# Performance work log

Measured on AMD Instinct MI355X. Metric: run time of the kernel, lower is better.

## Reference

```python
import jax, jax.numpy as jnp
import numpy as np

B, N, D = 8, 2048, 3
HIDDEN = (64, 128, 256)
LATENT = 128


def _layernorm(x, scale, bias, eps=1e-6):
    mu = jnp.mean(x, axis=-1, keepdims=True)
    var = jnp.mean((x - mu) ** 2, axis=-1, keepdims=True)
    return (x - mu) / jnp.sqrt(var + eps) * scale + bias


def setup_inputs() -> dict:
    key = jax.random.key(0)
    ks = jax.random.split(key, 8)
    inp = {
        "x": jax.random.normal(ks[0], (B, N, D), dtype=jnp.float32),
        "mask": jnp.ones((B, N), dtype=jnp.float32),
    }
    in_d = D
    for i, d in enumerate(HIDDEN):
        inp[f"W{i}"] = (jax.random.normal(ks[1 + i], (in_d, d), dtype=jnp.float32)
                        / np.float32(np.sqrt(in_d)))
        inp[f"b{i}"] = jnp.zeros((d,), dtype=jnp.float32)
        inp[f"g{i}"] = jnp.ones((d,), dtype=jnp.float32)
        inp[f"be{i}"] = jnp.zeros((d,), dtype=jnp.float32)
        in_d = d
    inp["Wz"] = (jax.random.normal(ks[5], (in_d, LATENT), dtype=jnp.float32)
                 / np.float32(np.sqrt(in_d)))
    inp["bz"] = jnp.zeros((LATENT,), dtype=jnp.float32)
    return inp


def reference(x, mask, W0, b0, g0, be0, W1, b1, g1, be1, W2, b2, g2, be2, Wz, bz):
    m = mask[..., None]                                   # (B, N, 1)
    count = jnp.sum(m, axis=1)                            # (B, 1)
    centroid = jnp.sum(x * m, axis=1, keepdims=True) / jnp.maximum(count, 1.0)[:, None, :]
    xc = x - centroid                                     # (B, N, D)

    # Pairwise squared distances; attention depends only on coordinates,
    # so it is identical for every layer -> compute once.
    diff = xc[:, :, None, :] - xc[:, None, :, :]          # (B, N, N, D)
    dist = jnp.sum(diff * diff, axis=-1)                  # (B, N, N)
    attn = jax.nn.softmax(-dist, axis=-1)                 # (B, N, N)

    h = xc
    for W, b, g, be in ((W0, b0, g0, be0), (W1, b1, g1, be1), (W2, b2, g2, be2)):
        h_agg = jnp.einsum('bij,bjd->bid', attn, h)       # weighted aggregation
        h = h_agg @ W + b
        h = _layernorm(h, g, be)
        h = jax.nn.swish(h)

    # Invariant readout: masked mean pool then Dense(latent)
    global_feat = jnp.sum(h * m, axis=1) / jnp.maximum(count, 1.0)
    z = global_feat @ Wz + bz                             # (B, latent)
    return z
```

## Files before the change

### kernel.cpp

```cpp
#include <hip/hip_runtime.h>
#include <hip/hip_bf16.h>

#define BATCH 8
#define NPTS 2048
#define LATENT 128

typedef __attribute__((ext_vector_type(8))) short short8;
typedef __attribute__((ext_vector_type(4))) float f32x4;

__device__ __forceinline__ ushort f2bf(float f) {
  unsigned int b = __float_as_uint(f);
  b += 0x7FFF + ((b >> 16) & 1);
  return (ushort)(b >> 16);
}

typedef unsigned int __attribute__((address_space(1))) gas_uint;
typedef unsigned int __attribute__((address_space(3))) las_uint;
__device__ __forceinline__ void gl_lds16(const void* g, void* l) {
  __builtin_amdgcn_global_load_lds((const gas_uint*)g, (las_uint*)l, 16, 0, 0);
}

#define L2E 1.4426950408889634f
#define SC2 1.6986436f

__global__ __launch_bounds__(256) void prep_kernel(const float* __restrict__ x,
    const float* __restrict__ mask, float4* __restrict__ pnt) {
  const int b = blockIdx.x;
  const int tid = threadIdx.x;
  const float* xb = x + (size_t)b * NPTS * 3;
  const float* mb = mask + (size_t)b * NPTS;
  float s0 = 0.f, s1 = 0.f, s2 = 0.f, c = 0.f;
  for (int n = tid; n < NPTS; n += 256) {
    float m = mb[n];
    s0 += xb[n * 3 + 0] * m;
    s1 += xb[n * 3 + 1] * m;
    s2 += xb[n * 3 + 2] * m;
    c += m;
  }
  __shared__ float red[4][256];
  red[0][tid] = s0; red[1][tid] = s1; red[2][tid] = s2; red[3][tid] = c;
  __syncthreads();
  for (int off = 128; off > 0; off >>= 1) {
    if (tid < off) {
      red[0][tid] += red[0][tid + off];
      red[1][tid] += red[1][tid + off];
      red[2][tid] += red[2][tid + off];
      red[3][tid] += red[3][tid + off];
    }
    __syncthreads();
  }
  const float cnt = fmaxf(red[3][0], 1.0f);
  const float c0 = red[0][0] / cnt, c1 = red[1][0] / cnt, c2 = red[2][0] / cnt;
  float4* pb = pnt + (size_t)b * NPTS;
  for (int n = tid; n < NPTS; n += 256) {
    const float a0 = xb[n * 3 + 0] - c0;
    const float a1 = xb[n * 3 + 1] - c1;
    const float a2 = xb[n * 3 + 2] - c2;
    pb[n] = make_float4(a0 * SC2, a1 * SC2, a2 * SC2,
                        -(a0 * a0 + a1 * a1 + a2 * a2) * L2E);
  }
}

__global__ __launch_bounds__(256) void wtrans_kernel(const float* __restrict__ W,
    ushort* __restrict__ WT, int K, int N) {
  __shared__ ushort s[64][72];
  const int tid = threadIdx.x;
  const int n0 = blockIdx.x * 64, k0 = blockIdx.y * 64;
  for (int i = tid; i < 64 * 64; i += 256) {
    const int kl = i >> 6, nl = i & 63;
    s[kl][nl] = f2bf(W[(size_t)(k0 + kl) * N + n0 + nl]);
  }
  __syncthreads();
  for (int i = tid; i < 64 * 64; i += 256) {
    const int nl = i >> 6, kl = i & 63;
    WT[(size_t)(n0 + nl) * K + k0 + kl] = s[kl][nl];
  }
}

__global__ __launch_bounds__(256) void agg3_kernel(const float4* __restrict__ pnt,
    float* __restrict__ hagg0) {
  const int b = blockIdx.y;
  const int i0 = blockIdx.x * 64;
  const int tid = threadIdx.x;
  const int il = tid & 63, part = tid >> 6;
  const float4* pb = pnt + (size_t)b * NPTS;
  const float4 pi = pb[i0 + il];
  float a0 = 0.f, a1 = 0.f, a2 = 0.f, dn = 0.f;
#pragma unroll 8
  for (int j = part * 512; j < part * 512 + 512; j++) {
    const float4 pj = pb[j];
    float arg = pi.w + pj.w;
    arg = fmaf(pi.x, pj.x, arg);
    arg = fmaf(pi.y, pj.y, arg);
    arg = fmaf(pi.z, pj.z, arg);
    const float w = __builtin_amdgcn_exp2f(arg);
    a0 = fmaf(w, pj.x, a0);
    a1 = fmaf(w, pj.y, a1);
    a2 = fmaf(w, pj.z, a2);
    dn += w;
  }
  __shared__ float4 sred[64][4];
  sred[il][part] = make_float4(a0, a1, a2, dn);
  __syncthreads();
  if (tid < 64) {
    const float4 r0 = sred[tid][0], r1 = sred[tid][1];
    const float4 r2 = sred[tid][2], r3 = sred[tid][3];
    const float A0 = (r0.x + r1.x) + (r2.x + r3.x);
    const float A1 = (r0.y + r1.y) + (r2.y + r3.y);
    const float A2 = (r0.z + r1.z) + (r2.z + r3.z);
    const float DN = (r0.w + r1.w) + (r2.w + r3.w);
    const float inv = 1.0f / (DN * SC2);
    float* op = hagg0 + ((size_t)b * NPTS + i0 + tid) * 3;
    op[0] = A0 * inv; op[1] = A1 * inv; op[2] = A2 * inv;
  }
}

__global__ __launch_bounds__(256) void mlp0_kernel(
    const float* __restrict__ in0, const float* __restrict__ W,
    const float* __restrict__ bias, const float* __restrict__ g,
    const float* __restrict__ be, ushort* __restrict__ hout) {
  constexpr int DIN = 3, DOUT = 64;
  const int tid = threadIdx.x;
  const int wv = tid >> 6, lane = tid & 63;
  const int r0 = blockIdx.x * 16;
  __shared__ float srow[16 * DIN];
  if (tid < 16 * DIN) srow[tid] = in0[(size_t)r0 * DIN + tid];
  __syncthreads();

  float o[4];
  const float bv = bias[lane];
#pragma unroll
  for (int r = 0; r < 4; r++) o[r] = bv;
#pragma unroll
  for (int k = 0; k < DIN; k++) {
    const float wk = W[(size_t)k * DOUT + lane];
#pragma unroll
    for (int r = 0; r < 4; r++)
      o[r] = fmaf(srow[(wv * 4 + r) * DIN + k], wk, o[r]);
  }
  __shared__ ushort lt[16][DOUT];
#pragma unroll
  for (int r = 0; r < 4; r++) {
    float m1 = o[r], m2 = o[r] * o[r];
#pragma unroll
    for (int off = 32; off > 0; off >>= 1) {
      m1 += __shfl_xor(m1, off, 64);
      m2 += __shfl_xor(m2, off, 64);
    }
    const float mu = m1 / DOUT;
    const float var = m2 / DOUT - mu * mu;
    const float rstd = rsqrtf(var + 1e-6f);
    const float v = (o[r] - mu) * rstd * g[lane] + be[lane];
    const float act = v / (1.0f + __expf(-v));
    lt[wv * 4 + r][lane] = f2bf(act);
  }
  __syncthreads();
  if (tid < DOUT) {
    ushort tmp[16];
#pragma unroll
    for (int r = 0; r < 16; r++) tmp[r] = lt[r][tid];
    const int bb = r0 / NPTS;
    const int nn = r0 % NPTS;
    ushort* dst = hout + ((size_t)bb * DOUT + tid) * NPTS + nn;
    *(uint4*)dst = *(uint4*)&tmp[0];
    *(uint4*)(dst + 8) = *(uint4*)&tmp[8];
  }
}

template <int DIN, int DOUT, bool POOL, int MINW>
__global__ __launch_bounds__(256, MINW) void fused_layer(
    const float4* __restrict__ pnt, const ushort* __restrict__ hT,
    const ushort* __restrict__ WT, const float* __restrict__ bias,
    const float* __restrict__ g, const float* __restrict__ be,
    ushort* __restrict__ hout, const float* __restrict__ mask,
    float* __restrict__ partial) {
  constexpr int NT = DIN / 16;
  constexpr int HALF = NPTS / 2;
  constexpr int TILES = HALF / 64;
  constexpr int NCOL = DOUT / 32;
  constexpr int PS = DIN + 8;
  constexpr int PN = DIN + 4;
  constexpr int SHT_B = 2 * 2 * DIN * 64 * 2;
  constexpr int SPNT_B = 2 * 2 * 64 * 16;
  constexpr int LOOP_B = SHT_B + SPNT_B;
  constexpr int SNUM_B = 4 * 32 * PN * 4;
  constexpr int OFF_SDEN = SNUM_B;
  constexpr int OFF_SINV = OFF_SDEN + 512;
  constexpr int OFF_SSTAT = OFF_SINV + 128;
  constexpr int OFF_SROW = OFF_SSTAT + 512;
  constexpr int EPI_B = OFF_SROW + 32 * PS * 2;
  constexpr int SMEM_B = LOOP_B > EPI_B ? LOOP_B : EPI_B;
  __shared__ __align__(16) char smem[SMEM_B];
  ushort* sht = (ushort*)smem;
  float4* spnt = (float4*)(smem + SHT_B);

  const int b = blockIdx.y;
  const int i0 = blockIdx.x * 32;
  const int tid = threadIdx.x;
  const int wv = tid >> 6, lane = tid & 63;
  const int h = wv >> 1;
  const int u = wv & 1;
  const int m = lane & 15, q = lane >> 4;
  const float4* pb = pnt + (size_t)b * NPTS;
  const ushort* hb = hT + (size_t)b * DIN * NPTS;

  const float4 pi0 = pb[i0 + m];
  const float4 pi1 = pb[i0 + 16 + m];

  f32x4 acc0[NT], acc1[NT];
#pragma unroll
  for (int nt = 0; nt < NT; nt++)
#pragma unroll
    for (int e = 0; e < 4; e++) { acc0[nt][e] = 0.f; acc1[nt][e] = 0.f; }
  float dacc0 = 0.f, dacc1 = 0.f;

  constexpr int NCH = (2 * DIN / 8) / 4;
  const int srow8 = lane >> 3;
  const int scsrc = (lane & 7) ^ srow8;
  const int jsw = ((lane & 7) << 3) | (lane >> 3);

  auto stage = [&](int t, int bf) {
    const int jb = t * 64;
#pragma unroll
    for (int i = 0; i < NCH; i++) {
      const int idx = wv * NCH + i;
      const int h2 = idx / (2 * NCH);
      const int oct = idx % (2 * NCH);
      const int row = oct * 8 + srow8;
      gl_lds16(hb + (size_t)row * NPTS + h2 * HALF + jb + scsrc * 8,
               sht + ((size_t)(bf * 2 + h2) * DIN + oct * 8) * 64);
    }
    if (wv == 0) {
#pragma unroll
      for (int h2 = 0; h2 < 2; h2++)
        gl_lds16(pb + h2 * HALF + jb + jsw, spnt + (bf * 2 + h2) * 64);
    }
  };

  stage(0, 0);
  __syncthreads();
  for (int t = 0; t < TILES; t++) {
    const int bf = t & 1;
    if (t + 1 < TILES) stage(t + 1, bf ^ 1);
    short8 af0, af1;
#pragma unroll
    for (int jj = 0; jj < 8; jj++) {
      const float4 pj = spnt[(bf * 2 + h) * 64 + ((jj << 3) | (u * 4 + q))];
      float a0 = pi0.w + pj.w;
      a0 = fmaf(pi0.x, pj.x, a0);
      a0 = fmaf(pi0.y, pj.y, a0);
      a0 = fmaf(pi0.z, pj.z, a0);
      float a1 = pi1.w + pj.w;
      a1 = fmaf(pi1.x, pj.x, a1);
      a1 = fmaf(pi1.y, pj.y, a1);
      a1 = fmaf(pi1.z, pj.z, a1);
      const float w0 = __builtin_amdgcn_exp2f(a0);
      const float w1 = __builtin_amdgcn_exp2f(a1);
      dacc0 += w0; dacc1 += w1;
      af0[jj] = (short)f2bf(w0);
      af1[jj] = (short)f2bf(w1);
    }
#pragma unroll
    for (int nt = 0; nt < NT; nt++) {
      const int d = nt * 16 + m;
      const short8 bfr = *(const short8*)
          &sht[((size_t)(bf * 2 + h) * DIN + d) * 64 + (((u * 4 + q) ^ (m & 7)) << 3)];
      acc0[nt] = __builtin_amdgcn_mfma_f32_16x16x32_bf16(af0, bfr, acc0[nt], 0, 0, 0);
      acc1[nt] = __builtin_amdgcn_mfma_f32_16x16x32_bf16(af1, bfr, acc1[nt], 0, 0, 0);
    }
    __syncthreads();
  }

  float* snum = (float*)smem;
  float* sden = (float*)(smem + OFF_SDEN);
  float* sinv = (float*)(smem + OFF_SINV);
  float* sstat = (float*)(smem + OFF_SSTAT);
  ushort* srow = (ushort*)(smem + OFF_SROW);

  dacc0 += __shfl_xor(dacc0, 16, 64);
  dacc0 += __shfl_xor(dacc0, 32, 64);
  dacc1 += __shfl_xor(dacc1, 16, 64);
  dacc1 += __shfl_xor(dacc1, 32, 64);
  if (q == 0) {
    sden[wv * 32 + m] = dacc0;
    sden[wv * 32 + 16 + m] = dacc1;
  }
#pragma unroll
  for (int nt = 0; nt < NT; nt++)
#pragma unroll
    for (int r = 0; r < 4; r++) {
      snum[(wv * 32 + q * 4 + r) * PN + nt * 16 + m] = acc0[nt][r];
      snum[(wv * 32 + 16 + q * 4 + r) * PN + nt * 16 + m] = acc1[nt][r];
    }
  __syncthreads();
  if (tid < 32)
    sinv[tid] = 1.0f / ((sden[tid] + sden[32 + tid]) + (sden[64 + tid] + sden[96 + tid]));
  __syncthreads();
  for (int idx = tid; idx < 32 * DIN; idx += 256) {
    const int r = idx / DIN, c = idx % DIN;
    const float s = ((snum[r * PN + c] + snum[32 * PN + r * PN + c]) +
                     (snum[64 * PN + r * PN + c] + snum[96 * PN + r * PN + c])) * sinv[r];
    srow[r * PS + c] = f2bf(s);
  }
  __syncthreads();

  const int rg2 = wv & 1, ch = wv >> 1;
  short8 afrag[DIN / 32];
#pragma unroll
  for (int kt = 0; kt < DIN / 32; kt++)
    afrag[kt] = *(const short8*)&srow[(rg2 * 16 + m) * PS + kt * 32 + q * 8];
  f32x4 oacc[NCOL];
#pragma unroll
  for (int c = 0; c < NCOL; c++)
#pragma unroll
    for (int e = 0; e < 4; e++) oacc[c][e] = 0.f;
#pragma unroll
  for (int c = 0; c < NCOL; c++) {
    const int n0 = (ch * NCOL + c) * 16;
#pragma unroll
    for (int kt = 0; kt < DIN / 32; kt++) {
      const short8 bfrag = *(const short8*)(WT + (size_t)(n0 + m) * DIN + kt * 32 + q * 8);
      oacc[c] = __builtin_amdgcn_mfma_f32_16x16x32_bf16(afrag[kt], bfrag, oacc[c], 0, 0, 0);
    }
  }

  float bcol[NCOL];
#pragma unroll
  for (int c = 0; c < NCOL; c++) bcol[c] = bias[(ch * NCOL + c) * 16 + m];
#pragma unroll
  for (int r = 0; r < 4; r++) {
    float m1 = 0.f, m2 = 0.f;
#pragma unroll
    for (int c = 0; c < NCOL; c++) {
      const float v = oacc[c][r] + bcol[c];
      m1 += v; m2 += v * v;
    }
#pragma unroll
    for (int off = 8; off > 0; off >>= 1) {
      m1 += __shfl_xor(m1, off, 64);
      m2 += __shfl_xor(m2, off, 64);
    }
    if (m == 0) {
      const int row = rg2 * 16 + q * 4 + r;
      sstat[(row * 2 + ch) * 2 + 0] = m1;
      sstat[(row * 2 + ch) * 2 + 1] = m2;
    }
  }
  __syncthreads();

  ushort* lt = (ushort*)smem;
  float* sp = (float*)smem;
  float pacc[NCOL];
  if (POOL) {
#pragma unroll
    for (int c = 0; c < NCOL; c++) pacc[c] = 0.f;
  }
#pragma unroll
  for (int r = 0; r < 4; r++) {
    const int row = rg2 * 16 + q * 4 + r;
    const float m1 = sstat[(row * 2 + 0) * 2 + 0] + sstat[(row * 2 + 1) * 2 + 0];
    const float m2 = sstat[(row * 2 + 0) * 2 + 1] + sstat[(row * 2 + 1) * 2 + 1];
    const float mu = m1 / DOUT;
    const float rstd = rsqrtf(m2 / DOUT - mu * mu + 1e-6f);
    float mval = 0.f;
    if (POOL) mval = mask[(size_t)b * NPTS + i0 + row];
#pragma unroll
    for (int c = 0; c < NCOL; c++) {
      const int dco = (ch * NCOL + c) * 16 + m;
      const float v = (oacc[c][r] + bcol[c] - mu) * rstd * g[dco] + be[dco];
      const float act = v / (1.0f + __expf(-v));
      if (POOL) pacc[c] = fmaf(act, mval, pacc[c]);
      else lt[row * DOUT + dco] = f2bf(act);
    }
  }
  if (POOL) {
#pragma unroll
    for (int c = 0; c < NCOL; c++) {
      float v = pacc[c];
      v += __shfl_xor(v, 16, 64);
      v += __shfl_xor(v, 32, 64);
      if (q == 0) sp[rg2 * DOUT + (ch * NCOL + c) * 16 + m] = v;
    }
    __syncthreads();
    if (tid < DOUT)
      partial[((size_t)b * (NPTS / 32) + blockIdx.x) * DOUT + tid] =
          sp[tid] + sp[DOUT + tid];
  } else {
    __syncthreads();
    if (tid < DOUT) {
      ushort tmp[32];
#pragma unroll
      for (int r = 0; r < 32; r++) tmp[r] = lt[r * DOUT + tid];
      ushort* dst = hout + ((size_t)b * DOUT + tid) * NPTS + i0;
#pragma unroll
      for (int c = 0; c < 4; c++)
        *(uint4*)(dst + c * 8) = *(uint4*)&tmp[c * 8];
    }
  }
}

__global__ __launch_bounds__(256) void readout_kernel(
    const float* __restrict__ partial, const float* __restrict__ mask,
    const float* __restrict__ Wz, const float* __restrict__ bz,
    float* __restrict__ out) {
  const int b = blockIdx.x;
  const int tid = threadIdx.x;
  const float* pb = partial + (size_t)b * (NPTS / 32) * 256;
  float s0 = 0.f, s1 = 0.f, s2 = 0.f, s3 = 0.f;
#pragma unroll 4
  for (int p = 0; p < NPTS / 32; p += 4) {
    s0 += pb[(size_t)(p + 0) * 256 + tid];
    s1 += pb[(size_t)(p + 1) * 256 + tid];
    s2 += pb[(size_t)(p + 2) * 256 + tid];
    s3 += pb[(size_t)(p + 3) * 256 + tid];
  }
  const float s = (s0 + s1) + (s2 + s3);
  const float* mb = mask + (size_t)b * NPTS;
  float c = 0.f;
  for (int n = tid; n < NPTS; n += 256) c += mb[n];
  __shared__ float red[256];
  red[tid] = c;
  __syncthreads();
  for (int off = 128; off > 0; off >>= 1) {
    if (tid < off) red[tid] += red[tid + off];
    __syncthreads();
  }
  const float cnt = fmaxf(red[0], 1.0f);
  __shared__ float gf[256];
  gf[tid] = s / cnt;
  __syncthreads();
  if (tid < LATENT) {
    float z = bz[tid];
#pragma unroll 4
    for (int d = 0; d < 256; d++) z += gf[d] * Wz[(size_t)d * LATENT + tid];
    out[(size_t)b * LATENT + tid] = z;
  }
}

extern "C" void kernel_launch(void* const* d_in, const int* in_sizes, int n_in,
                              void* d_out, int out_size, void* d_ws, size_t ws_size,
                              hipStream_t stream) {
  const float* x    = (const float*)d_in[0];
  const float* mask = (const float*)d_in[1];
  const float* W0   = (const float*)d_in[2];
  const float* b0   = (const float*)d_in[3];
  const float* g0   = (const float*)d_in[4];
  const float* be0  = (const float*)d_in[5];
  const float* W1   = (const float*)d_in[6];
  const float* b1   = (const float*)d_in[7];
  const float* g1   = (const float*)d_in[8];
  const float* be1  = (const float*)d_in[9];
  const float* W2   = (const float*)d_in[10];
  const float* b2   = (const float*)d_in[11];
  const float* g2   = (const float*)d_in[12];
  const float* be2  = (const float*)d_in[13];
  const float* Wz   = (const float*)d_in[14];
  const float* bz   = (const float*)d_in[15];
  float* out = (float*)d_out;

  char* ws = (char*)d_ws;
  float4* pnt     = (float4*)(ws);
  float*  hagg0   = (float*)(ws + 262144);
  ushort* h1T     = (ushort*)(ws + 458752);
  ushort* h2T     = (ushort*)(ws + 2555904);
  float*  partial = (float*)(ws + 6750208);
  ushort* WT1     = (ushort*)(ws + 7274496);
  ushort* WT2     = (ushort*)(ws + 7290880);

  prep_kernel<<<dim3(BATCH), dim3(256), 0, stream>>>(x, mask, pnt);
  wtrans_kernel<<<dim3(128 / 64, 64 / 64), dim3(256), 0, stream>>>(W1, WT1, 64, 128);
  wtrans_kernel<<<dim3(256 / 64, 128 / 64), dim3(256), 0, stream>>>(W2, WT2, 128, 256);

  agg3_kernel<<<dim3(NPTS / 64, BATCH), dim3(256), 0, stream>>>(pnt, hagg0);
  mlp0_kernel<<<dim3(BATCH * NPTS / 16), dim3(256), 0, stream>>>(
      hagg0, W0, b0, g0, be0, h1T);

  fused_layer<64, 128, false, 3><<<dim3(NPTS / 32, BATCH), dim3(256), 0, stream>>>(
      pnt, h1T, WT1, b1, g1, be1, h2T, nullptr, nullptr);

  fused_layer<128, 256, true, 2><<<dim3(NPTS / 32, BATCH), dim3(256), 0, stream>>>(
      pnt, h2T, WT2, b2, g2, be2, nullptr, mask, partial);

  readout_kernel<<<dim3(BATCH), dim3(256), 0, stream>>>(partial, mask, Wz, bz, out);
}
```

Before: 210.2 us.

## Merge setup kernels, fuse layer0 aggregation with MLP, double row tile in fused layers

Merges the centroid prep and both weight transposes into one launch. Fuses the 3-dim attention aggregation with the first dense, layernorm and swish layer so the intermediate no longer goes through global memory. Fused layers now use 512-thread blocks that handle 64 query rows, so two row groups share each streamed key/feature tile. This halves the grid and the number of partial sums, but puts fewer blocks in flight and serialises the cross-wave reduction over four sync rounds.

```diff
diff --git a/kernel.cpp b/kernel.cpp
--- a/kernel.cpp
+++ b/kernel.cpp
@@ -23,10 +23,35 @@
 #define L2E 1.4426950408889634f
 #define SC2 1.6986436f
 
-__global__ __launch_bounds__(256) void prep_kernel(const float* __restrict__ x,
-    const float* __restrict__ mask, float4* __restrict__ pnt) {
-  const int b = blockIdx.x;
+__device__ __forceinline__ void wtrans_tile(const float* __restrict__ W,
+    ushort* __restrict__ WT, int K, int N, int n0, int k0, int tid) {
+  __shared__ ushort s[64][72];
+  for (int i = tid; i < 64 * 64; i += 256) {
+    const int kl = i >> 6, nl = i & 63;
+    s[kl][nl] = f2bf(W[(size_t)(k0 + kl) * N + n0 + nl]);
+  }
+  __syncthreads();
+  for (int i = tid; i < 64 * 64; i += 256) {
+    const int nl = i >> 6, kl = i & 63;
+    WT[(size_t)(n0 + nl) * K + k0 + kl] = s[kl][nl];
+  }
+}
+
+__global__ __launch_bounds__(256) void setup_kernel(const float* __restrict__ x,
+    const float* __restrict__ mask, float4* __restrict__ pnt,
+    const float* __restrict__ W1, ushort* __restrict__ WT1,
+    const float* __restrict__ W2, ushort* __restrict__ WT2) {
+  const int bid = blockIdx.x;
   const int tid = threadIdx.x;
+  if (bid >= 8) {
+    if (bid < 10) wtrans_tile(W1, WT1, 64, 128, (bid - 8) * 64, 0, tid);
+    else {
+      const int idx = bid - 10;
+      wtrans_tile(W2, WT2, 128, 256, (idx & 3) * 64, (idx >> 2) * 64, tid);
+    }
+    return;
+  }
+  const int b = bid;
   const float* xb = x + (size_t)b * NPTS * 3;
   const float* mb = mask + (size_t)b * NPTS;
   float s0 = 0.f, s1 = 0.f, s2 = 0.f, c = 0.f;
@@ -61,24 +86,10 @@
   }
 }
 
-__global__ __launch_bounds__(256) void wtrans_kernel(const float* __restrict__ W,
-    ushort* __restrict__ WT, int K, int N) {
-  __shared__ ushort s[64][72];
-  const int tid = threadIdx.x;
-  const int n0 = blockIdx.x * 64, k0 = blockIdx.y * 64;
-  for (int i = tid; i < 64 * 64; i += 256) {
-    const int kl = i >> 6, nl = i & 63;
-    s[kl][nl] = f2bf(W[(size_t)(k0 + kl) * N + n0 + nl]);
-  }
-  __syncthreads();
-  for (int i = tid; i < 64 * 64; i += 256) {
-    const int nl = i >> 6, kl = i & 63;
-    WT[(size_t)(n0 + nl) * K + k0 + kl] = s[kl][nl];
-  }
-}
-
-__global__ __launch_bounds__(256) void agg3_kernel(const float4* __restrict__ pnt,
-    float* __restrict__ hagg0) {
+__global__ __launch_bounds__(512) void layer0_kernel(
+    const float4* __restrict__ pnt, const float* __restrict__ W,
+    const float* __restrict__ bias, const float* __restrict__ g,
+    const float* __restrict__ be, ushort* __restrict__ hout) {
   const int b = blockIdx.y;
   const int i0 = blockIdx.x * 64;
   const int tid = threadIdx.x;
@@ -87,7 +98,7 @@
   const float4 pi = pb[i0 + il];
   float a0 = 0.f, a1 = 0.f, a2 = 0.f, dn = 0.f;
 #pragma unroll 8
-  for (int j = part * 512; j < part * 512 + 512; j++) {
+  for (int j = part * 256; j < part * 256 + 256; j++) {
     const float4 pj = pb[j];
     float arg = pi.w + pj.w;
     arg = fmaf(pi.x, pj.x, arg);
@@ -99,76 +110,60 @@
     a2 = fmaf(w, pj.z, a2);
     dn += w;
   }
-  __shared__ float4 sred[64][4];
-  sred[il][part] = make_float4(a0, a1, a2, dn);
+  __shared__ float4 sred[8][64];
+  __shared__ float srow[64 * 3];
+  __shared__ ushort lt[64][64];
+  sred[part][il] = make_float4(a0, a1, a2, dn);
   __syncthreads();
   if (tid < 64) {
-    const float4 r0 = sred[tid][0], r1 = sred[tid][1];
-    const float4 r2 = sred[tid][2], r3 = sred[tid][3];
-    const float A0 = (r0.x + r1.x) + (r2.x + r3.x);
-    const float A1 = (r0.y + r1.y) + (r2.y + r3.y);
-    const float A2 = (r0.z + r1.z) + (r2.z + r3.z);
-    const float DN = (r0.w + r1.w) + (r2.w + r3.w);
+    float A0 = 0.f, A1 = 0.f, A2 = 0.f, DN = 0.f;
+#pragma unroll
+    for (int p = 0; p < 8; p++) {
+      const float4 r = sred[p][tid];
+      A0 += r.x; A1 += r.y; A2 += r.z; DN += r.w;
+    }
     const float inv = 1.0f / (DN * SC2);
-    float* op = hagg0 + ((size_t)b * NPTS + i0 + tid) * 3;
-    op[0] = A0 * inv; op[1] = A1 * inv; op[2] = A2 * inv;
-  }
-}
-
-__global__ __launch_bounds__(256) void mlp0_kernel(
-    const float* __restrict__ in0, const float* __restrict__ W,
-    const float* __restrict__ bias, const float* __restrict__ g,
-    const float* __restrict__ be, ushort* __restrict__ hout) {
-  constexpr int DIN = 3, DOUT = 64;
-  const int tid = threadIdx.x;
+    srow[tid * 3 + 0] = A0 * inv;
+    srow[tid * 3 + 1] = A1 * inv;
+    srow[tid * 3 + 2] = A2 * inv;
+  }
+  __syncthreads();
   const int wv = tid >> 6, lane = tid & 63;
-  const int r0 = blockIdx.x * 16;
-  __shared__ float srow[16 * DIN];
-  if (tid < 16 * DIN) srow[tid] = in0[(size_t)r0 * DIN + tid];
-  __syncthreads();
-
-  float o[4];
-  const float bv = bias[lane];
-#pragma unroll
-  for (int r = 0; r < 4; r++) o[r] = bv;
-#pragma unroll
-  for (int k = 0; k < DIN; k++) {
-    const float wk = W[(size_t)k * DOUT + lane];
-#pragma unroll
-    for (int r = 0; r < 4; r++)
-      o[r] = fmaf(srow[(wv * 4 + r) * DIN + k], wk, o[r]);
-  }
-  __shared__ ushort lt[16][DOUT];
-#pragma unroll
-  for (int r = 0; r < 4; r++) {
-    float m1 = o[r], m2 = o[r] * o[r];
+  const float w0c = W[lane], w1c = W[64 + lane], w2c = W[128 + lane];
+  const float gv = g[lane], bev = be[lane], bv = bias[lane];
+#pragma unroll
+  for (int r = 0; r < 8; r++) {
+    const int row = wv * 8 + r;
+    float o = bv;
+    o = fmaf(srow[row * 3 + 0], w0c, o);
+    o = fmaf(srow[row * 3 + 1], w1c, o);
+    o = fmaf(srow[row * 3 + 2], w2c, o);
+    float m1 = o, m2 = o * o;
 #pragma unroll
     for (int off = 32; off > 0; off >>= 1) {
       m1 += __shfl_xor(m1, off, 64);
       m2 += __shfl_xor(m2, off, 64);
     }
-    const float mu = m1 / DOUT;
-    const float var = m2 / DOUT - mu * mu;
-    const float rstd = rsqrtf(var + 1e-6f);
-    const float v = (o[r] - mu) * rstd * g[lane] + be[lane];
+    const float mu = m1 / 64.f;
+    const float rstd = rsqrtf(m2 / 64.f - mu * mu + 1e-6f);
+    const float v = (o - mu) * rstd * gv + bev;
     const float act = v / (1.0f + __expf(-v));
-    lt[wv * 4 + r][lane] = f2bf(act);
-  }
-  __syncthreads();
-  if (tid < DOUT) {
-    ushort tmp[16];
-#pragma unroll
-    for (int r = 0; r < 16; r++) tmp[r] = lt[r][tid];
-    const int bb = r0 / NPTS;
-    const int nn = r0 % NPTS;
-    ushort* dst = hout + ((size_t)bb * DOUT + tid) * NPTS + nn;
-    *(uint4*)dst = *(uint4*)&tmp[0];
-    *(uint4*)(dst + 8) = *(uint4*)&tmp[8];
-  }
-}
-
-template <int DIN, int DOUT, bool POOL, int MINW>
-__global__ __launch_bounds__(256, MINW) void fused_layer(
+    lt[row][lane] = f2bf(act);
+  }
+  __syncthreads();
+  if (tid < 64) {
+    ushort tmp[64];
+#pragma unroll
+    for (int r = 0; r < 64; r++) tmp[r] = lt[r][tid];
+    ushort* dst = hout + ((size_t)b * 64 + tid) * NPTS + i0;
+#pragma unroll
+    for (int c = 0; c < 8; c++)
+      *(uint4*)(dst + c * 8) = *(uint4*)&tmp[c * 8];
+  }
+}
+
+template <int DIN, int DOUT, bool POOL>
+__global__ __launch_bounds__(512, 2) void fused_layer(
     const float4* __restrict__ pnt, const ushort* __restrict__ hT,
     const ushort* __restrict__ WT, const float* __restrict__ bias,
     const float* __restrict__ g, const float* __restrict__ be,
@@ -183,29 +178,30 @@
   constexpr int SHT_B = 2 * 2 * DIN * 64 * 2;
   constexpr int SPNT_B = 2 * 2 * 64 * 16;
   constexpr int LOOP_B = SHT_B + SPNT_B;
-  constexpr int SNUM_B = 4 * 32 * PN * 4;
-  constexpr int OFF_SDEN = SNUM_B;
-  constexpr int OFF_SINV = OFF_SDEN + 512;
-  constexpr int OFF_SSTAT = OFF_SINV + 128;
-  constexpr int OFF_SROW = OFF_SSTAT + 512;
-  constexpr int EPI_B = OFF_SROW + 32 * PS * 2;
+  constexpr int SNUM_B = 64 * PN * 4;
+  constexpr int OFF_SROW = SNUM_B;
+  constexpr int OFF_SDEN = OFF_SROW + 64 * PS * 2;
+  constexpr int OFF_SINV = OFF_SDEN + 256;
+  constexpr int OFF_SSTAT = OFF_SINV + 256;
+  constexpr int EPI_B = OFF_SSTAT + 1024;
   constexpr int SMEM_B = LOOP_B > EPI_B ? LOOP_B : EPI_B;
   __shared__ __align__(16) char smem[SMEM_B];
   ushort* sht = (ushort*)smem;
   float4* spnt = (float4*)(smem + SHT_B);
 
   const int b = blockIdx.y;
-  const int i0 = blockIdx.x * 32;
+  const int i0 = blockIdx.x * 64;
   const int tid = threadIdx.x;
   const int wv = tid >> 6, lane = tid & 63;
-  const int h = wv >> 1;
+  const int h = (wv >> 1) & 1;
   const int u = wv & 1;
+  const int rg = wv >> 2;
   const int m = lane & 15, q = lane >> 4;
   const float4* pb = pnt + (size_t)b * NPTS;
   const ushort* hb = hT + (size_t)b * DIN * NPTS;
 
-  const float4 pi0 = pb[i0 + m];
-  const float4 pi1 = pb[i0 + 16 + m];
+  const float4 pi0 = pb[i0 + rg * 32 + m];
+  const float4 pi1 = pb[i0 + rg * 32 + 16 + m];
 
   f32x4 acc0[NT], acc1[NT];
 #pragma unroll
@@ -214,7 +210,7 @@
     for (int e = 0; e < 4; e++) { acc0[nt][e] = 0.f; acc1[nt][e] = 0.f; }
   float dacc0 = 0.f, dacc1 = 0.f;
 
-  constexpr int NCH = (2 * DIN / 8) / 4;
+  constexpr int NCH = DIN / 32;
   const int srow8 = lane >> 3;
   const int scsrc = (lane & 7) ^ srow8;
   const int jsw = ((lane & 7) << 3) | (lane >> 3);
@@ -224,8 +220,8 @@
 #pragma unroll
     for (int i = 0; i < NCH; i++) {
       const int idx = wv * NCH + i;
-      const int h2 = idx / (2 * NCH);
-      const int oct = idx % (2 * NCH);
+      const int h2 = idx / (DIN / 8);
+      const int oct = idx % (DIN / 8);
       const int row = oct * 8 + srow8;
       gl_lds16(hb + (size_t)row * NPTS + h2 * HALF + jb + scsrc * 8,
                sht + ((size_t)(bf * 2 + h2) * DIN + oct * 8) * 64);
@@ -272,39 +268,55 @@
   }
 
   float* snum = (float*)smem;
+  ushort* srow = (ushort*)(smem + OFF_SROW);
   float* sden = (float*)(smem + OFF_SDEN);
   float* sinv = (float*)(smem + OFF_SINV);
   float* sstat = (float*)(smem + OFF_SSTAT);
-  ushort* srow = (ushort*)(smem + OFF_SROW);
 
   dacc0 += __shfl_xor(dacc0, 16, 64);
   dacc0 += __shfl_xor(dacc0, 32, 64);
   dacc1 += __shfl_xor(dacc1, 16, 64);
   dacc1 += __shfl_xor(dacc1, 32, 64);
-  if (q == 0) {
-    sden[wv * 32 + m] = dacc0;
-    sden[wv * 32 + 16 + m] = dacc1;
-  }
-#pragma unroll
-  for (int nt = 0; nt < NT; nt++)
-#pragma unroll
-    for (int r = 0; r < 4; r++) {
-      snum[(wv * 32 + q * 4 + r) * PN + nt * 16 + m] = acc0[nt][r];
-      snum[(wv * 32 + 16 + q * 4 + r) * PN + nt * 16 + m] = acc1[nt][r];
-    }
-  __syncthreads();
-  if (tid < 32)
-    sinv[tid] = 1.0f / ((sden[tid] + sden[32 + tid]) + (sden[64 + tid] + sden[96 + tid]));
-  __syncthreads();
-  for (int idx = tid; idx < 32 * DIN; idx += 256) {
-    const int r = idx / DIN, c = idx % DIN;
-    const float s = ((snum[r * PN + c] + snum[32 * PN + r * PN + c]) +
-                     (snum[64 * PN + r * PN + c] + snum[96 * PN + r * PN + c])) * sinv[r];
-    srow[r * PS + c] = f2bf(s);
-  }
-  __syncthreads();
-
-  const int rg2 = wv & 1, ch = wv >> 1;
+  const int quarter = wv & 3;
+  for (int p = 0; p < 4; p++) {
+    if (quarter == p) {
+      if (p == 0) {
+#pragma unroll
+        for (int nt = 0; nt < NT; nt++)
+#pragma unroll
+          for (int r = 0; r < 4; r++) {
+            snum[(rg * 32 + q * 4 + r) * PN + nt * 16 + m] = acc0[nt][r];
+            snum[(rg * 32 + 16 + q * 4 + r) * PN + nt * 16 + m] = acc1[nt][r];
+          }
+        if (q == 0) {
+          sden[rg * 32 + m] = dacc0;
+          sden[rg * 32 + 16 + m] = dacc1;
+        }
+      } else {
+#pragma unroll
+        for (int nt = 0; nt < NT; nt++)
+#pragma unroll
+          for (int r = 0; r < 4; r++) {
+            snum[(rg * 32 + q * 4 + r) * PN + nt * 16 + m] += acc0[nt][r];
+            snum[(rg * 32 + 16 + q * 4 + r) * PN + nt * 16 + m] += acc1[nt][r];
+          }
+        if (q == 0) {
+          sden[rg * 32 + m] += dacc0;
+          sden[rg * 32 + 16 + m] += dacc1;
+        }
+      }
+    }
+    __syncthreads();
+  }
+  if (tid < 64) sinv[tid] = 1.0f / sden[tid];
+  __syncthreads();
+  for (int idx = tid; idx < 64 * DIN; idx += 512) {
+    const int r = idx / DIN, c = idx & (DIN - 1);
+    srow[r * PS + c] = f2bf(snum[r * PN + c] * sinv[r]);
+  }
+  __syncthreads();
+
+  const int rg2 = wv >> 1, ch = wv & 1;
   short8 afrag[DIN / 32];
 #pragma unroll
   for (int kt = 0; kt < DIN / 32; kt++)
@@ -383,17 +395,17 @@
     }
     __syncthreads();
     if (tid < DOUT)
-      partial[((size_t)b * (NPTS / 32) + blockIdx.x) * DOUT + tid] =
-          sp[tid] + sp[DOUT + tid];
+      partial[((size_t)b * (NPTS / 64) + blockIdx.x) * DOUT + tid] =
+          (sp[tid] + sp[DOUT + tid]) + (sp[2 * DOUT + tid] + sp[3 * DOUT + tid]);
   } else {
     __syncthreads();
     if (tid < DOUT) {
-      ushort tmp[32];
-#pragma unroll
-      for (int r = 0; r < 32; r++) tmp[r] = lt[r * DOUT + tid];
+      ushort tmp[64];
+#pragma unroll
+      for (int r = 0; r < 64; r++) tmp[r] = lt[r * DOUT + tid];
       ushort* dst = hout + ((size_t)b * DOUT + tid) * NPTS + i0;
 #pragma unroll
-      for (int c = 0; c < 4; c++)
+      for (int c = 0; c < 8; c++)
         *(uint4*)(dst + c * 8) = *(uint4*)&tmp[c * 8];
     }
   }
@@ -405,10 +417,10 @@
     float* __restrict__ out) {
   const int b = blockIdx.x;
   const int tid = threadIdx.x;
-  const float* pb = partial + (size_t)b * (NPTS / 32) * 256;
+  const float* pb = partial + (size_t)b * (NPTS / 64) * 256;
   float s0 = 0.f, s1 = 0.f, s2 = 0.f, s3 = 0.f;
-#pragma unroll 4
-  for (int p = 0; p < NPTS / 32; p += 4) {
+#pragma unroll
+  for (int p = 0; p < NPTS / 64; p += 4) {
     s0 += pb[(size_t)(p + 0) * 256 + tid];
     s1 += pb[(size_t)(p + 1) * 256 + tid];
     s2 += pb[(size_t)(p + 2) * 256 + tid];
@@ -460,25 +472,21 @@
 
   char* ws = (char*)d_ws;
   float4* pnt     = (float4*)(ws);
-  float*  hagg0   = (float*)(ws + 262144);
-  ushort* h1T     = (ushort*)(ws + 458752);
-  ushort* h2T     = (ushort*)(ws + 2555904);
-  float*  partial = (float*)(ws + 6750208);
-  ushort* WT1     = (ushort*)(ws + 7274496);
-  ushort* WT2     = (ushort*)(ws + 7290880);
-
-  prep_kernel<<<dim3(BATCH), dim3(256), 0, stream>>>(x, mask, pnt);
-  wtrans_kernel<<<dim3(128 / 64, 64 / 64), dim3(256), 0, stream>>>(W1, WT1, 64, 128);
-  wtrans_kernel<<<dim3(256 / 64, 128 / 64), dim3(256), 0, stream>>>(W2, WT2, 128, 256);
-
-  agg3_kernel<<<dim3(NPTS / 64, BATCH), dim3(256), 0, stream>>>(pnt, hagg0);
-  mlp0_kernel<<<dim3(BATCH * NPTS / 16), dim3(256), 0, stream>>>(
-      hagg0, W0, b0, g0, be0, h1T);
-
-  fused_layer<64, 128, false, 3><<<dim3(NPTS / 32, BATCH), dim3(256), 0, stream>>>(
+  ushort* h1T     = (ushort*)(ws + 262144);
+  ushort* h2T     = (ushort*)(ws + 2359296);
+  float*  partial = (float*)(ws + 6553600);
+  ushort* WT1     = (ushort*)(ws + 6815744);
+  ushort* WT2     = (ushort*)(ws + 6832128);
+
+  setup_kernel<<<dim3(18), dim3(256), 0, stream>>>(x, mask, pnt, W1, WT1, W2, WT2);
+
+  layer0_kernel<<<dim3(NPTS / 64, BATCH), dim3(512), 0, stream>>>(
+      pnt, W0, b0, g0, be0, h1T);
+
+  fused_layer<64, 128, false><<<dim3(NPTS / 64, BATCH), dim3(512), 0, stream>>>(
       pnt, h1T, WT1, b1, g1, be1, h2T, nullptr, nullptr);
 
-  fused_layer<128, 256, true, 2><<<dim3(NPTS / 32, BATCH), dim3(256), 0, stream>>>(
+  fused_layer<128, 256, true><<<dim3(NPTS / 64, BATCH), dim3(512), 0, stream>>>(
       pnt, h2T, WT2, b2, g2, be2, nullptr, mask, partial);
 
   readout_kernel<<<dim3(BATCH), dim3(256), 0, stream>>>(partial, mask, Wz, bz, out);
```

New measurement: 196.8 us. 1.07x faster.
